# Performance work log

Measured on AMD Instinct MI355X. Metric: run time of the kernel, lower is better.

Reference implementation:

```python
import jax, jax.numpy as jnp
import numpy as np

D_IN, D, K, N_CLASSES = 384, 512, 6, 2
SCALE = D ** (-0.5)

def _linear_params(key, fan_in, fan_out):
    kw, kb = jax.random.split(key)
    w = jax.random.normal(kw, (fan_in, fan_out), jnp.float32) * 0.02
    b = jax.random.normal(kb, (fan_out,), jnp.float32) * 0.01
    return w, b

def setup_inputs() -> dict:
    key = jax.random.key(0)
    ks = jax.random.split(key, 10)
    x = jax.random.normal(ks[0], (16384, D_IN), jnp.float32)
    fc1_w, fc1_b = _linear_params(ks[1], D_IN, D)
    wh_w, wh_b = _linear_params(ks[2], D, D)
    wt_w, wt_b = _linear_params(ks[3], D, D)
    lin1_w, lin1_b = _linear_params(ks[4], D, D)
    lin2_w, lin2_b = _linear_params(ks[5], D, D)
    att1_w, att1_b = _linear_params(ks[6], D, D // 2)
    att2_w, att2_b = _linear_params(ks[7], D // 2, 1)
    ln_g = jnp.ones((D,), jnp.float32)
    ln_b = jnp.zeros((D,), jnp.float32)
    fc_w, fc_b = _linear_params(ks[8], D, N_CLASSES)
    return dict(x=x, fc1_w=fc1_w, fc1_b=fc1_b, wh_w=wh_w, wh_b=wh_b,
                wt_w=wt_w, wt_b=wt_b, lin1_w=lin1_w, lin1_b=lin1_b,
                lin2_w=lin2_w, lin2_b=lin2_b, att1_w=att1_w, att1_b=att1_b,
                att2_w=att2_w, att2_b=att2_b, ln_g=ln_g, ln_b=ln_b,
                fc_w=fc_w, fc_b=fc_b)

def _forward(x, fc1_w, fc1_b, wh_w, wh_b, wt_w, wt_b, lin1_w, lin1_b,
             lin2_w, lin2_b, att1_w, att1_b, att2_w, att2_b, ln_g, ln_b,
             fc_w, fc_b):
    lrelu = jax.nn.leaky_relu  # slope 0.01, matches nn.LeakyReLU default
    h = lrelu(x @ fc1_w + fc1_b)                    # [N, D]
    h = (h + h.mean(axis=0, keepdims=True)) * 0.5
    e_h = h @ wh_w + wh_b                           # [N, D]
    e_t = h @ wt_w + wt_b                           # [N, D]
    attn_logit = (e_h * SCALE) @ e_t.T              # [N, N]
    topk_w, topk_i = jax.lax.top_k(attn_logit, K)   # [N, K]
    Nb = e_t[topk_i]                                # gather neighbors [N, K, D]
    p = jax.nn.softmax(topk_w, axis=-1)             # [N, K]
    eh_r = p[..., None] * Nb + (1.0 - p)[..., None] * e_h[:, None, :]
    gate = jnp.tanh(e_h[:, None, :] + eh_r)         # [N, K, D]
    # faithful to torch.einsum('ijkl,ijkm->ijk', Nb, gate): product of sums
    ka_w = Nb.sum(axis=-1) * gate.sum(axis=-1)      # [N, K]
    ka_p = jax.nn.softmax(ka_w, axis=-1)
    e_Nh = jnp.einsum('nk,nkd->nd', ka_p, Nb)       # [N, D]
    sum_emb = lrelu((e_h + e_Nh) @ lin1_w + lin1_b)
    bi_emb = lrelu((e_h * e_Nh) @ lin2_w + lin2_b)
    emb = sum_emb + bi_emb                          # [N, D] (dropout=eval, identity)
    # GlobalAttention readout
    a = lrelu(emb @ att1_w + att1_b) @ att2_w + att2_b  # [N, 1]
    g = jax.nn.softmax(a, axis=0)
    pooled = (g * emb).sum(axis=0, keepdims=True)   # [1, D]
    mu = pooled.mean(axis=-1, keepdims=True)
    var = pooled.var(axis=-1, keepdims=True)
    normed = (pooled - mu) * jax.lax.rsqrt(var + 1e-5) * ln_g + ln_b
    logits = normed @ fc_w + fc_b                   # [1, n_classes]
    return logits

def reference(x, fc1_w, fc1_b, wh_w, wh_b, wt_w, wt_b, lin1_w, lin1_b,
              lin2_w, lin2_b, att1_w, att1_b, att2_w, att2_b, ln_g, ln_b,
              fc_w, fc_b):
    logits = _forward(x, fc1_w, fc1_b, wh_w, wh_b, wt_w, wt_b, lin1_w, lin1_b,
                      lin2_w, lin2_b, att1_w, att1_b, att2_w, att2_b,
                      ln_g, ln_b, fc_w, fc_b)
    y_prob = jax.nn.softmax(logits, axis=-1)
    return logits, y_prob
```

## Files before the change

kernel.cpp:

```cpp
#include <hip/hip_runtime.h>
#include <math.h>

#define NROWS 16384
#define DIN   384
#define DIM   512
#define KSEL  6
#define NSPLIT 4
#define COLS_PER_SPLIT (NROWS / NSPLIT)
#define ATT_SCALE 0.044194173824159216f

typedef unsigned short u16;
typedef __attribute__((ext_vector_type(8))) short bf16x8;
typedef __attribute__((ext_vector_type(16))) float f32x16;

static __device__ __forceinline__ float lrelu_f(float v) {
  return v > 0.f ? v : 0.01f * v;
}

static __device__ __forceinline__ u16 f2bf(float f) {
  unsigned u = __float_as_uint(f);
  unsigned r = (u + 0x7FFFu + ((u >> 16) & 1u)) >> 16;
  return (u16)r;
}

static __device__ __forceinline__ void sbar() {
  asm volatile("" ::: "memory");
  __builtin_amdgcn_s_barrier();
  asm volatile("" ::: "memory");
}

static __device__ __forceinline__ void wconv_body(const float* W, u16* Wt,
                                                  int K, int N, int t) {
  if (t >= K * N) return;
  int k = t / N, n = t - k * N;
  Wt[(size_t)n * K + k] = f2bf(W[t]);
}

__global__ __launch_bounds__(256)
void prep(const float* __restrict__ X, u16* __restrict__ Xb,
          const float* __restrict__ fc1_w, u16* __restrict__ fc1t,
          const float* __restrict__ wh_w, u16* __restrict__ wht,
          const float* __restrict__ wt_w, u16* __restrict__ wtt,
          const float* __restrict__ lin1_w, u16* __restrict__ lin1t,
          const float* __restrict__ lin2_w, u16* __restrict__ lin2t,
          const float* __restrict__ att1_w, u16* __restrict__ att1t) {
  const int b = blockIdx.x, tid = threadIdx.x;
  if (b < 3072) {
    int i = b * 256 + tid;
    const float4* p = (const float4*)X + (size_t)i * 2;
    float4 a = p[0], c = p[1];
    uint4 o;
    o.x = f2bf(a.x) | ((unsigned)f2bf(a.y) << 16);
    o.y = f2bf(a.z) | ((unsigned)f2bf(a.w) << 16);
    o.z = f2bf(c.x) | ((unsigned)f2bf(c.y) << 16);
    o.w = f2bf(c.z) | ((unsigned)f2bf(c.w) << 16);
    ((uint4*)Xb)[i] = o;
  } else if (b < 3840) {
    wconv_body(fc1_w, fc1t, 384, 512, (b - 3072) * 256 + tid);
  } else if (b < 4864) {
    wconv_body(wh_w, wht, 512, 512, (b - 3840) * 256 + tid);
  } else if (b < 5888) {
    wconv_body(wt_w, wtt, 512, 512, (b - 4864) * 256 + tid);
  } else if (b < 6912) {
    wconv_body(lin1_w, lin1t, 512, 512, (b - 5888) * 256 + tid);
  } else if (b < 7936) {
    wconv_body(lin2_w, lin2t, 512, 512, (b - 6912) * 256 + tid);
  } else {
    wconv_body(att1_w, att1t, 512, 256, (b - 7936) * 256 + tid);
  }
}

__global__ __launch_bounds__(256)
void colsum_partial(const float* __restrict__ H, float* __restrict__ part) {
  int col = blockIdx.x * 64 + (threadIdx.x & 63);
  int sub = threadIdx.x >> 6;
  int rEnd = blockIdx.y * 512 + 512;
  float s = 0.f;
  for (int r = blockIdx.y * 512 + sub; r < rEnd; r += 4)
    s += H[(size_t)r * DIM + col];
  __shared__ float sh[4][64];
  sh[sub][threadIdx.x & 63] = s;
  __syncthreads();
  if (threadIdx.x < 64) {
    float tot = sh[0][threadIdx.x] + sh[1][threadIdx.x] +
                sh[2][threadIdx.x] + sh[3][threadIdx.x];
    part[(size_t)blockIdx.y * DIM + col] = tot;
  }
}

__global__ void finalize_mean(const float* __restrict__ part,
                              float* __restrict__ mean) {
  int c = threadIdx.x;
  float s = 0.f;
  for (int j = 0; j < 32; j++) s += part[j * DIM + c];
  mean[c] = s * (1.0f / NROWS);
}

__global__ __launch_bounds__(256)
void h_fix_bf(const float* __restrict__ H0, const float* __restrict__ mean,
              u16* __restrict__ Hb) {
  int idx = blockIdx.x * 256 + threadIdx.x;
  int c = (idx * 8) & (DIM - 1);
  const float4* p = (const float4*)H0 + (size_t)idx * 2;
  float4 a = p[0], b = p[1];
  float4 m0 = *(const float4*)(mean + c);
  float4 m1 = *(const float4*)(mean + c + 4);
  a.x = (a.x + m0.x) * 0.5f; a.y = (a.y + m0.y) * 0.5f;
  a.z = (a.z + m0.z) * 0.5f; a.w = (a.w + m0.w) * 0.5f;
  b.x = (b.x + m1.x) * 0.5f; b.y = (b.y + m1.y) * 0.5f;
  b.z = (b.z + m1.z) * 0.5f; b.w = (b.w + m1.w) * 0.5f;
  uint4 o;
  o.x = f2bf(a.x) | ((unsigned)f2bf(a.y) << 16);
  o.y = f2bf(a.z) | ((unsigned)f2bf(a.w) << 16);
  o.z = f2bf(b.x) | ((unsigned)f2bf(b.y) << 16);
  o.w = f2bf(b.z) | ((unsigned)f2bf(b.w) << 16);
  ((uint4*)Hb)[idx] = o;
}

template<int ACT, int ACCUM, int STOREBF>
__global__ __launch_bounds__(256, 2)
void gemm_bf16(const u16* __restrict__ A, const u16* __restrict__ Wt,
               const float* __restrict__ bias, float* __restrict__ C,
               u16* __restrict__ Cb, float bscale, int K, int N) {
  __shared__ char lds[65536];
  const int tid = threadIdx.x;
  const int w = tid >> 6, l = tid & 63;
  const int l31 = l & 31, lh = l >> 5, lh16 = lh << 4;
  const int qg = w & 1, ng = w >> 1;
  const int swz = (l31 & 7) << 4;
  const int rowBase = blockIdx.y * 128;
  const int colBase = blockIdx.x * 128;
  const int nsteps = K >> 6;

  f32x16 z;
  #pragma unroll
  for (int i = 0; i < 16; i++) z[i] = 0.f;
  f32x16 acc00 = z, acc01 = z, acc10 = z, acc11 = z;

#define GSTAGE(buf_, kc_) do { \
    const int r_ = tid >> 3, j_ = tid & 7; \
    const int js_ = ((j_ ^ (r_ & 7)) << 3); \
    const u16* as_ = A + (size_t)rowBase * K + (kc_); \
    const u16* ws_ = Wt + (size_t)colBase * K + (kc_); \
    char* ab_ = lds + (buf_) * 16384; \
    char* wb_ = lds + 32768 + (buf_) * 16384; \
    _Pragma("unroll") \
    for (int p_ = 0; p_ < 4; ++p_) { \
      __builtin_amdgcn_global_load_lds( \
        (const __attribute__((address_space(1))) void*)(as_ + (size_t)(r_ + 32 * p_) * K + js_), \
        (__attribute__((address_space(3))) void*)(ab_ + w * 1024 + p_ * 4096), 16, 0, 0); \
      __builtin_amdgcn_global_load_lds( \
        (const __attribute__((address_space(1))) void*)(ws_ + (size_t)(r_ + 32 * p_) * K + js_), \
        (__attribute__((address_space(3))) void*)(wb_ + w * 1024 + p_ * 4096), 16, 0, 0); \
    } \
  } while (0)

  GSTAGE(0, 0);
  asm volatile("s_waitcnt vmcnt(0)" ::: "memory");
  sbar();
  #pragma unroll 1
  for (int s = 0; s < nsteps; ++s) {
    const int cur = s & 1;
    if (s + 1 < nsteps) GSTAGE(cur ^ 1, (s + 1) * 64);
    __builtin_amdgcn_sched_barrier(0);
    const char* ab = lds + cur * 16384;
    const char* wb = lds + 32768 + cur * 16384;
    __builtin_amdgcn_s_setprio(1);
    #pragma unroll
    for (int s4 = 0; s4 < 4; ++s4) {
      const int off = (s4 * 32 + lh16) ^ swz;
      bf16x8 am0 = *(const bf16x8*)(ab + (qg * 64 + l31) * 128 + off);
      bf16x8 am1 = *(const bf16x8*)(ab + (qg * 64 + 32 + l31) * 128 + off);
      bf16x8 wn0 = *(const bf16x8*)(wb + (ng * 64 + l31) * 128 + off);
      bf16x8 wn1 = *(const bf16x8*)(wb + (ng * 64 + 32 + l31) * 128 + off);
      acc00 = __builtin_amdgcn_mfma_f32_32x32x16_bf16(wn0, am0, acc00, 0, 0, 0);
      acc01 = __builtin_amdgcn_mfma_f32_32x32x16_bf16(wn1, am0, acc01, 0, 0, 0);
      acc10 = __builtin_amdgcn_mfma_f32_32x32x16_bf16(wn0, am1, acc10, 0, 0, 0);
      acc11 = __builtin_amdgcn_mfma_f32_32x32x16_bf16(wn1, am1, acc11, 0, 0, 0);
    }
    __builtin_amdgcn_s_setprio(0);
    asm volatile("s_waitcnt vmcnt(0)" ::: "memory");
    sbar();
  }
#undef GSTAGE

  float* Ls = (float*)lds;
  {
    const int m0 = qg * 64 + l31;
    const int k0 = (m0 & 7) << 2;
    #pragma unroll
    for (int r = 0; r < 16; ++r) {
      const int nd = ng * 64 + (r & 3) + 8 * (r >> 2) + 4 * lh;
      Ls[m0 * 128 + (nd ^ k0)] = acc00[r];
      Ls[m0 * 128 + ((nd + 32) ^ k0)] = acc01[r];
      Ls[(m0 + 32) * 128 + (nd ^ k0)] = acc10[r];
      Ls[(m0 + 32) * 128 + ((nd + 32) ^ k0)] = acc11[r];
    }
  }
  sbar();
  #pragma unroll
  for (int p = 0; p < 16; ++p) {
    int idx = tid + 256 * p;
    int m = idx >> 5, c4 = (idx & 31) << 2;
    float4 v = *(const float4*)&Ls[m * 128 + (c4 ^ ((m & 7) << 2))];
    int col = colBase + c4;
    float4 bv = *(const float4*)&bias[col];
    v.x += bv.x; v.y += bv.y; v.z += bv.z; v.w += bv.w;
    if (ACT) {
      v.x = lrelu_f(v.x); v.y = lrelu_f(v.y);
      v.z = lrelu_f(v.z); v.w = lrelu_f(v.w);
    }
    size_t o = (size_t)(rowBase + m) * N + col;
    if (ACCUM) {
      float4 c0 = *(const float4*)&C[o];
      v.x += c0.x; v.y += c0.y; v.z += c0.z; v.w += c0.w;
    }
    *(float4*)&C[o] = v;
    if (STOREBF) {
      ushort4 q;
      q.x = f2bf(v.x * bscale); q.y = f2bf(v.y * bscale);
      q.z = f2bf(v.z * bscale); q.w = f2bf(v.w * bscale);
      *(ushort4*)&Cb[o] = q;
    }
  }
}

#define T6(tv, tix, vv, cc) do { float v_ = (vv); \
  if (v_ > tv[5]) { tv[5] = v_; tix[5] = (cc); \
    if (tv[5] > tv[4]) { float t=tv[4];tv[4]=tv[5];tv[5]=t; int q=tix[4];tix[4]=tix[5];tix[5]=q; } \
    if (tv[4] > tv[3]) { float t=tv[3];tv[3]=tv[4];tv[4]=t; int q=tix[3];tix[3]=tix[4];tix[4]=q; } \
    if (tv[3] > tv[2]) { float t=tv[2];tv[2]=tv[3];tv[3]=t; int q=tix[2];tix[2]=tix[3];tix[3]=q; } \
    if (tv[2] > tv[1]) { float t=tv[1];tv[1]=tv[2];tv[2]=t; int q=tix[1];tix[1]=tix[2];tix[2]=q; } \
    if (tv[1] > tv[0]) { float t=tv[0];tv[0]=tv[1];tv[1]=t; int q=tix[0];tix[0]=tix[1];tix[1]=q; } \
  } } while (0)

__global__ __launch_bounds__(256, 2)
void attn_topk_mfma(const u16* __restrict__ EHb, const u16* __restrict__ ETb,
                    float* __restrict__ TWp, int* __restrict__ TIp) {
  __shared__ char lds[49152];
  const int tid = threadIdx.x;
  const int w = tid >> 6, l = tid & 63;
  const int l31 = l & 31, lh = l >> 5;

  const int bid = blockIdx.x;
  const int xcd = bid & 7;
  const int split = xcd & 3;
  const int rowBase = ((xcd >> 2) * 64 + (bid >> 3)) * 128;
  const int qrow = rowBase + w * 32 + l31;

  bf16x8 areg[32];
  {
    const u16* ap = EHb + (size_t)qrow * DIM + lh * 8;
    #pragma unroll
    for (int ks = 0; ks < 32; ++ks)
      areg[ks] = *(const bf16x8*)(ap + ks * 16);
  }

  f32x16 z;
  #pragma unroll
  for (int i = 0; i < 16; i++) z[i] = 0.f;
  f32x16 acc0 = z, acc1 = z;

  float tv[KSEL]; int tix[KSEL];
  #pragma unroll
  for (int k = 0; k < KSEL; k++) { tv[k] = -INFINITY; tix[k] = 0x7fffffff; }

#define STAGE(bufi_, ph_) do { \
    const int ct_ = (ph_) >> 2, kc_ = (ph_) & 3; \
    char* db_ = lds + (bufi_) * 16384; \
    const u16* bs_ = ETb + (size_t)(split * COLS_PER_SPLIT + ct_ * 64) * DIM + kc_ * 128; \
    _Pragma("unroll") \
    for (int p_ = 0; p_ < 4; ++p_) { \
      const int c_ = (w * 4 + p_) * 64 + l; \
      const int rn_ = c_ >> 4; \
      const int js_ = ((c_ & 15) ^ (rn_ & 15)) << 3; \
      __builtin_amdgcn_global_load_lds( \
        (const __attribute__((address_space(1))) void*)(bs_ + (size_t)rn_ * DIM + js_), \
        (__attribute__((address_space(3))) void*)(db_ + (w * 4 + p_) * 1024), 16, 0, 0); \
    } \
  } while (0)

  int bufr = 0;
  STAGE(0, 0);
  STAGE(1, 1);
  asm volatile("s_waitcnt vmcnt(4)" ::: "memory");

  #pragma unroll 1
  for (int ct = 0; ct < 64; ++ct) {
    #pragma unroll
    for (int kc = 0; kc < 4; ++kc) {
      sbar();
      const char* db = lds + bufr * 16384;
      __builtin_amdgcn_s_setprio(1);
      #pragma unroll
      for (int s = 0; s < 8; ++s) {
        const int j0 = ((s * 2 + lh) ^ (l31 & 15)) * 16;
        bf16x8 bn0 = *(const bf16x8*)(db + l31 * 256 + j0);
        const int r1 = 32 + l31;
        const int j1 = ((s * 2 + lh) ^ (r1 & 15)) * 16;
        bf16x8 bn1 = *(const bf16x8*)(db + r1 * 256 + j1);
        acc0 = __builtin_amdgcn_mfma_f32_32x32x16_bf16(bn0, areg[kc * 8 + s], acc0, 0, 0, 0);
        acc1 = __builtin_amdgcn_mfma_f32_32x32x16_bf16(bn1, areg[kc * 8 + s], acc1, 0, 0, 0);
      }
      __builtin_amdgcn_s_setprio(0);
      if (kc == 3) {
        const int cb = split * COLS_PER_SPLIT + ct * 64 + 4 * lh;
        #pragma unroll
        for (int r = 0; r < 16; ++r) {
          const int nd = cb + (r & 3) + 8 * (r >> 2);
          T6(tv, tix, acc0[r], nd);
          T6(tv, tix, acc1[r], nd + 32);
        }
        acc0 = z; acc1 = z;
      }
      __builtin_amdgcn_sched_barrier(0);
      {
        const int p = ct * 4 + kc;
        if (p + 2 < 256) {
          const int bs = (bufr >= 1) ? bufr - 1 : bufr + 2;
          STAGE(bs, p + 2);
        }
        if (p < 254) { asm volatile("s_waitcnt vmcnt(4)" ::: "memory"); }
        else         { asm volatile("s_waitcnt vmcnt(0)" ::: "memory"); }
      }
      bufr = (bufr == 2) ? 0 : bufr + 1;
    }
  }
#undef STAGE

  {
    float pv[KSEL]; int pi[KSEL];
    #pragma unroll
    for (int k = 0; k < KSEL; k++) {
      pv[k] = __shfl_xor(tv[k], 32);
      pi[k] = __shfl_xor(tix[k], 32);
    }
    #pragma unroll
    for (int k = 0; k < KSEL; k++) {
      float cv = pv[k]; int ci = pi[k];
      if ((cv > tv[5]) || (cv == tv[5] && ci < tix[5])) {
        tv[5] = cv; tix[5] = ci;
        if ((tv[5] > tv[4]) || (tv[5] == tv[4] && tix[5] < tix[4])) {
          float t = tv[4]; tv[4] = tv[5]; tv[5] = t;
          int q = tix[4]; tix[4] = tix[5]; tix[5] = q; }
        if ((tv[4] > tv[3]) || (tv[4] == tv[3] && tix[4] < tix[3])) {
          float t = tv[3]; tv[3] = tv[4]; tv[4] = t;
          int q = tix[3]; tix[3] = tix[4]; tix[4] = q; }
        if ((tv[3] > tv[2]) || (tv[3] == tv[2] && tix[3] < tix[2])) {
          float t = tv[2]; tv[2] = tv[3]; tv[3] = t;
          int q = tix[2]; tix[2] = tix[3]; tix[3] = q; }
        if ((tv[2] > tv[1]) || (tv[2] == tv[1] && tix[2] < tix[1])) {
          float t = tv[1]; tv[1] = tv[2]; tv[2] = t;
          int q = tix[1]; tix[1] = tix[2]; tix[2] = q; }
        if ((tv[1] > tv[0]) || (tv[1] == tv[0] && tix[1] < tix[0])) {
          float t = tv[0]; tv[0] = tv[1]; tv[1] = t;
          int q = tix[0]; tix[0] = tix[1]; tix[1] = q; }
      }
    }
  }
  if (lh == 0) {
    size_t o = ((size_t)split * NROWS + qrow) * KSEL;
    #pragma unroll
    for (int k = 0; k < KSEL; k++) { TWp[o + k] = tv[k]; TIp[o + k] = tix[k]; }
  }
}

__global__ __launch_bounds__(256)
void neighbor_kernel(const float* __restrict__ EH, const float* __restrict__ ET,
                     const float* __restrict__ TWp, const int* __restrict__ TIp,
                     u16* __restrict__ SINb, u16* __restrict__ BINb) {
  const int lane = threadIdx.x & 63;
  const int row = blockIdx.x * 4 + (threadIdx.x >> 6);
  const float* eh = EH + (size_t)row * DIM;
  float ehv[8];
  #pragma unroll
  for (int u = 0; u < 8; u++) ehv[u] = eh[u * 64 + lane];

  float tw[KSEL]; int ti[KSEL];
  #pragma unroll
  for (int k = 0; k < KSEL; k++) { tw[k] = -INFINITY; ti[k] = 0x7fffffff; }
  #pragma unroll
  for (int s = 0; s < NSPLIT; s++) {
    size_t o = ((size_t)s * NROWS + row) * KSEL;
    #pragma unroll
    for (int k = 0; k < KSEL; k++) {
      float cv = TWp[o + k]; int ci = TIp[o + k];
      if ((cv > tw[5]) || (cv == tw[5] && ci < ti[5])) {
        tw[5] = cv; ti[5] = ci;
        if ((tw[5] > tw[4]) || (tw[5] == tw[4] && ti[5] < ti[4])) {
          float t = tw[4]; tw[4] = tw[5]; tw[5] = t;
          int q = ti[4]; ti[4] = ti[5]; ti[5] = q; }
        if ((tw[4] > tw[3]) || (tw[4] == tw[3] && ti[4] < ti[3])) {
          float t = tw[3]; tw[3] = tw[4]; tw[4] = t;
          int q = ti[3]; ti[3] = ti[4]; ti[4] = q; }
        if ((tw[3] > tw[2]) || (tw[3] == tw[2] && ti[3] < ti[2])) {
          float t = tw[2]; tw[2] = tw[3]; tw[3] = t;
          int q = ti[2]; ti[2] = ti[3]; ti[3] = q; }
        if ((tw[2] > tw[1]) || (tw[2] == tw[1] && ti[2] < ti[1])) {
          float t = tw[1]; tw[1] = tw[2]; tw[2] = t;
          int q = ti[1]; ti[1] = ti[2]; ti[2] = q; }
        if ((tw[1] > tw[0]) || (tw[1] == tw[0] && ti[1] < ti[0])) {
          float t = tw[0]; tw[0] = tw[1]; tw[1] = t;
          int q = ti[0]; ti[0] = ti[1]; ti[1] = q; }
      }
    }
  }

  float m = tw[0];
  #pragma unroll
  for (int k = 1; k < KSEL; k++) m = fmaxf(m, tw[k]);
  float p[KSEL], ps = 0.f;
  #pragma unroll
  for (int k = 0; k < KSEL; k++) { p[k] = expf(tw[k] - m); ps += p[k]; }
  float inv = 1.f / ps;
  #pragma unroll
  for (int k = 0; k < KSEL; k++) p[k] *= inv;

  float nb[KSEL][8];
  float kaw[KSEL];
  #pragma unroll
  for (int k = 0; k < KSEL; k++) {
    const float* et = ET + (size_t)ti[k] * DIM;
    float snb = 0.f, sg = 0.f;
    #pragma unroll
    for (int u = 0; u < 8; u++) {
      float nbv = et[u * 64 + lane];
      nb[k][u] = nbv;
      float ehr = p[k] * nbv + (1.f - p[k]) * ehv[u];
      float g = tanhf(ehv[u] + ehr);
      snb += nbv; sg += g;
    }
    #pragma unroll
    for (int off = 32; off > 0; off >>= 1) {
      snb += __shfl_xor(snb, off);
      sg  += __shfl_xor(sg, off);
    }
    kaw[k] = snb * sg;
  }
  float km = kaw[0];
  #pragma unroll
  for (int k = 1; k < KSEL; k++) km = fmaxf(km, kaw[k]);
  float kp[KSEL], ks = 0.f;
  #pragma unroll
  for (int k = 0; k < KSEL; k++) { kp[k] = expf(kaw[k] - km); ks += kp[k]; }
  float kinv = 1.f / ks;
  #pragma unroll
  for (int k = 0; k < KSEL; k++) kp[k] *= kinv;

  #pragma unroll
  for (int u = 0; u < 8; u++) {
    float enh = 0.f;
    #pragma unroll
    for (int k = 0; k < KSEL; k++) enh += kp[k] * nb[k][u];
    size_t o = (size_t)row * DIM + u * 64 + lane;
    SINb[o] = f2bf(ehv[u] + enh);
    BINb[o] = f2bf(ehv[u] * enh);
  }
}

__global__ __launch_bounds__(256)
void att2_kernel(const float* __restrict__ HID, const float* __restrict__ w2,
                 const float* __restrict__ b2, float* __restrict__ ASC) {
  const int lane = threadIdx.x & 63;
  const int row = blockIdx.x * 4 + (threadIdx.x >> 6);
  float4 hv = ((const float4*)(HID + (size_t)row * 256))[lane];
  float4 wv = ((const float4*)w2)[lane];
  float s = hv.x * wv.x + hv.y * wv.y + hv.z * wv.z + hv.w * wv.w;
  #pragma unroll
  for (int off = 32; off > 0; off >>= 1) s += __shfl_xor(s, off);
  if (lane == 0) ASC[row] = s + b2[0];
}

__global__ __launch_bounds__(1024)
void areduce(const float* __restrict__ ASC, float* __restrict__ stats) {
  __shared__ float sm[1024];
  int t = threadIdx.x;
  float m = -INFINITY;
  for (int i = t; i < NROWS; i += 1024) m = fmaxf(m, ASC[i]);
  sm[t] = m; __syncthreads();
  for (int s = 512; s > 0; s >>= 1) {
    if (t < s) sm[t] = fmaxf(sm[t], sm[t + s]);
    __syncthreads();
  }
  float mx = sm[0]; __syncthreads();
  float sum = 0.f;
  for (int i = t; i < NROWS; i += 1024) sum += expf(ASC[i] - mx);
  sm[t] = sum; __syncthreads();
  for (int s = 512; s > 0; s >>= 1) {
    if (t < s) sm[t] += sm[t + s];
    __syncthreads();
  }
  if (t == 0) { stats[0] = mx; stats[1] = sm[0]; }
}

__global__ __launch_bounds__(256)
void pooled_partial(const float* __restrict__ EMB, const float* __restrict__ ASC,
                    const float* __restrict__ stats, float* __restrict__ part) {
  int col = blockIdx.x * 64 + (threadIdx.x & 63);
  int sub = threadIdx.x >> 6;
  float mx = stats[0];
  int rEnd = blockIdx.y * 512 + 512;
  float s = 0.f;
  for (int r = blockIdx.y * 512 + sub; r < rEnd; r += 4)
    s += expf(ASC[r] - mx) * EMB[(size_t)r * DIM + col];
  __shared__ float sh[4][64];
  sh[sub][threadIdx.x & 63] = s;
  __syncthreads();
  if (threadIdx.x < 64) {
    float tot = sh[0][threadIdx.x] + sh[1][threadIdx.x] +
                sh[2][threadIdx.x] + sh[3][threadIdx.x];
    part[(size_t)blockIdx.y * DIM + col] = tot;
  }
}

__global__ __launch_bounds__(512)
void final_kernel(const float* __restrict__ part, const float* __restrict__ stats,
                  const float* __restrict__ ln_g, const float* __restrict__ ln_b,
                  const float* __restrict__ fc_w, const float* __restrict__ fc_b,
                  float* __restrict__ out) {
  __shared__ float sh[512];
  int t = threadIdx.x;
  float s = 0.f;
  for (int j = 0; j < 32; j++) s += part[j * DIM + t];
  float pooled = s / stats[1];
  sh[t] = pooled; __syncthreads();
  for (int off = 256; off > 0; off >>= 1) {
    if (t < off) sh[t] += sh[t + off];
    __syncthreads();
  }
  float mu = sh[0] * (1.f / DIM); __syncthreads();
  float dv = pooled - mu;
  sh[t] = dv * dv; __syncthreads();
  for (int off = 256; off > 0; off >>= 1) {
    if (t < off) sh[t] += sh[t + off];
    __syncthreads();
  }
  float var = sh[0] * (1.f / DIM); __syncthreads();
  float normed = dv * rsqrtf(var + 1e-5f) * ln_g[t] + ln_b[t];
  sh[t] = normed * fc_w[t * 2 + 0]; __syncthreads();
  for (int off = 256; off > 0; off >>= 1) {
    if (t < off) sh[t] += sh[t + off];
    __syncthreads();
  }
  float l0 = sh[0] + fc_b[0]; __syncthreads();
  sh[t] = normed * fc_w[t * 2 + 1]; __syncthreads();
  for (int off = 256; off > 0; off >>= 1) {
    if (t < off) sh[t] += sh[t + off];
    __syncthreads();
  }
  float l1 = sh[0] + fc_b[1];
  if (t == 0) {
    float mm = fmaxf(l0, l1);
    float e0 = expf(l0 - mm), e1 = expf(l1 - mm);
    float si = 1.f / (e0 + e1);
    out[0] = l0; out[1] = l1; out[2] = e0 * si; out[3] = e1 * si;
  }
}

extern "C" void kernel_launch(void* const* d_in, const int* in_sizes, int n_in,
                              void* d_out, int out_size, void* d_ws, size_t ws_size,
                              hipStream_t stream) {
  (void)in_sizes; (void)n_in; (void)out_size; (void)ws_size;
  const float* x      = (const float*)d_in[0];
  const float* fc1_w  = (const float*)d_in[1];
  const float* fc1_b  = (const float*)d_in[2];
  const float* wh_w   = (const float*)d_in[3];
  const float* wh_b   = (const float*)d_in[4];
  const float* wt_w   = (const float*)d_in[5];
  const float* wt_b   = (const float*)d_in[6];
  const float* lin1_w = (const float*)d_in[7];
  const float* lin1_b = (const float*)d_in[8];
  const float* lin2_w = (const float*)d_in[9];
  const float* lin2_b = (const float*)d_in[10];
  const float* att1_w = (const float*)d_in[11];
  const float* att1_b = (const float*)d_in[12];
  const float* att2_w = (const float*)d_in[13];
  const float* att2_b = (const float*)d_in[14];
  const float* ln_g   = (const float*)d_in[15];
  const float* ln_b   = (const float*)d_in[16];
  const float* fc_w   = (const float*)d_in[17];
  const float* fc_b   = (const float*)d_in[18];
  float* out = (float*)d_out;

  char* ws = (char*)d_ws;
  float* B0   = (float*)(ws);
  float* B1   = (float*)(ws + 33554432);
  float* B2   = (float*)(ws + 67108864);
  float* TWp  = (float*)(ws + 100663296);
  int*   TIp  = (int*)  (ws + 100663296 + 1572864);
  float* part = (float*)(ws + 100663296 + 3145728 + 786432);
  float* mean = (float*)(ws + 100663296 + 3145728 + 786432 + 65536);
  float* ascr = (float*)(ws + 100663296 + 3145728 + 786432 + 65536 + 2048);
  float* stats= (float*)(ws + 100663296 + 3145728 + 786432 + 65536 + 2048 + 65536);
  u16*   hb   = (u16*)(ws + 104732672);
  u16*   EHb  = (u16*)(ws + 104732672 + 16777216);
  u16*   ETb  = (u16*)(ws + 104732672 + 33554432);
  u16*   WT   = (u16*)(ws + 104732672 + 50331648);
  u16* fc1t = WT;
  u16* wht  = fc1t + 196608;
  u16* wtt  = wht + 262144;
  u16* lin1t= wtt + 262144;
  u16* lin2t= lin1t + 262144;
  u16* att1t= lin2t + 262144;
  u16* xb   = (u16*)B1;
  u16* sinb = EHb;
  u16* binb = ETb;
  u16* embb = hb;

  prep<<<8448, 256, 0, stream>>>(x, xb, fc1_w, fc1t, wh_w, wht, wt_w, wtt,
                                 lin1_w, lin1t, lin2_w, lin2t, att1_w, att1t);
  gemm_bf16<1,0,0><<<dim3(4,128), 256, 0, stream>>>(xb, fc1t, fc1_b, B0, nullptr, 1.f, 384, 512);
  colsum_partial<<<dim3(8,32), 256, 0, stream>>>(B0, part);
  finalize_mean<<<1, 512, 0, stream>>>(part, mean);
  h_fix_bf<<<4096, 256, 0, stream>>>(B0, mean, hb);
  gemm_bf16<0,0,1><<<dim3(4,128), 256, 0, stream>>>(hb, wht, wh_b, B1, EHb, ATT_SCALE, 512, 512);
  gemm_bf16<0,0,1><<<dim3(4,128), 256, 0, stream>>>(hb, wtt, wt_b, B2, ETb, 1.f, 512, 512);
  attn_topk_mfma<<<512, 256, 0, stream>>>(EHb, ETb, TWp, TIp);
  neighbor_kernel<<<4096, 256, 0, stream>>>(B1, B2, TWp, TIp, sinb, binb);
  gemm_bf16<1,0,0><<<dim3(4,128), 256, 0, stream>>>(sinb, lin1t, lin1_b, B2, nullptr, 1.f, 512, 512);
  gemm_bf16<1,1,1><<<dim3(4,128), 256, 0, stream>>>(binb, lin2t, lin2_b, B2, embb, 1.f, 512, 512);
  gemm_bf16<1,0,0><<<dim3(2,128), 256, 0, stream>>>(embb, att1t, att1_b, B0, nullptr, 1.f, 512, 256);
  att2_kernel<<<4096, 256, 0, stream>>>(B0, att2_w, att2_b, ascr);
  areduce<<<1, 1024, 0, stream>>>(ascr, stats);
  pooled_partial<<<dim3(8,32), 256, 0, stream>>>(B2, ascr, stats, part);
  final_kernel<<<1, 512, 0, stream>>>(part, stats, ln_g, ln_b, fc_w, fc_b, out);
}
```

Baseline: 602.8 us.

## Split top-k attention columns into eight chunks with double-buffered LDS

The attention/top-k kernel now divides each column split into two halves, doubling the grid to 1024 blocks. LDS staging drops from triple to double buffering (32 KB), and launch bounds ask for three blocks per CU to raise occupancy. Each block also remaps its row tile by XCD. The neighbor kernel merges eight partial top-k lists instead of four, and the partial buffers move into the free B0 region. In exchange, each block reloads its query rows for twice as many blocks, the prefetch depth shrinks to one stage with a full vmcnt wait per step, and 1024 blocks at three per CU may leave an uneven tail wave.

```diff
diff --git a/kernel.cpp b/kernel.cpp
--- a/kernel.cpp
+++ b/kernel.cpp
@@ -234,18 +234,23 @@
     if (tv[1] > tv[0]) { float t=tv[0];tv[0]=tv[1];tv[1]=t; int q=tix[0];tix[0]=tix[1];tix[1]=q; } \
   } } while (0)
 
-__global__ __launch_bounds__(256, 2)
+__global__ __launch_bounds__(256, 3)
 void attn_topk_mfma(const u16* __restrict__ EHb, const u16* __restrict__ ETb,
                     float* __restrict__ TWp, int* __restrict__ TIp) {
-  __shared__ char lds[49152];
+  __shared__ char lds[32768];
   const int tid = threadIdx.x;
   const int w = tid >> 6, l = tid & 63;
   const int l31 = l & 31, lh = l >> 5;
 
   const int bid = blockIdx.x;
   const int xcd = bid & 7;
-  const int split = xcd & 3;
-  const int rowBase = ((xcd >> 2) * 64 + (bid >> 3)) * 128;
+  const int rem = bid >> 3;
+  const int rowTileL = rem & 15;
+  const int sc = rem >> 4;
+  const int split = sc & 3;
+  const int ch = sc >> 2;
+  const int rowBase = (xcd * 16 + rowTileL) * 128;
+  const int colBase0 = split * COLS_PER_SPLIT + ch * 2048;
   const int qrow = rowBase + w * 32 + l31;
 
   bf16x8 areg[32];
@@ -268,7 +273,7 @@
 #define STAGE(bufi_, ph_) do { \
     const int ct_ = (ph_) >> 2, kc_ = (ph_) & 3; \
     char* db_ = lds + (bufi_) * 16384; \
-    const u16* bs_ = ETb + (size_t)(split * COLS_PER_SPLIT + ct_ * 64) * DIM + kc_ * 128; \
+    const u16* bs_ = ETb + (size_t)(colBase0 + ct_ * 64) * DIM + kc_ * 128; \
     _Pragma("unroll") \
     for (int p_ = 0; p_ < 4; ++p_) { \
       const int c_ = (w * 4 + p_) * 64 + l; \
@@ -280,17 +285,18 @@
     } \
   } while (0)
 
-  int bufr = 0;
   STAGE(0, 0);
-  STAGE(1, 1);
-  asm volatile("s_waitcnt vmcnt(4)" ::: "memory");
+  asm volatile("s_waitcnt vmcnt(0)" ::: "memory");
 
   #pragma unroll 1
-  for (int ct = 0; ct < 64; ++ct) {
+  for (int ct = 0; ct < 32; ++ct) {
     #pragma unroll
     for (int kc = 0; kc < 4; ++kc) {
+      const int p = ct * 4 + kc;
       sbar();
-      const char* db = lds + bufr * 16384;
+      if (p + 1 < 128) STAGE((p + 1) & 1, p + 1);
+      __builtin_amdgcn_sched_barrier(0);
+      const char* db = lds + (p & 1) * 16384;
       __builtin_amdgcn_s_setprio(1);
       #pragma unroll
       for (int s = 0; s < 8; ++s) {
@@ -304,7 +310,7 @@
       }
       __builtin_amdgcn_s_setprio(0);
       if (kc == 3) {
-        const int cb = split * COLS_PER_SPLIT + ct * 64 + 4 * lh;
+        const int cb = colBase0 + ct * 64 + 4 * lh;
         #pragma unroll
         for (int r = 0; r < 16; ++r) {
           const int nd = cb + (r & 3) + 8 * (r >> 2);
@@ -314,16 +320,7 @@
         acc0 = z; acc1 = z;
       }
       __builtin_amdgcn_sched_barrier(0);
-      {
-        const int p = ct * 4 + kc;
-        if (p + 2 < 256) {
-          const int bs = (bufr >= 1) ? bufr - 1 : bufr + 2;
-          STAGE(bs, p + 2);
-        }
-        if (p < 254) { asm volatile("s_waitcnt vmcnt(4)" ::: "memory"); }
-        else         { asm volatile("s_waitcnt vmcnt(0)" ::: "memory"); }
-      }
-      bufr = (bufr == 2) ? 0 : bufr + 1;
+      asm volatile("s_waitcnt vmcnt(0)" ::: "memory");
     }
   }
 #undef STAGE
@@ -359,7 +356,7 @@
     }
   }
   if (lh == 0) {
-    size_t o = ((size_t)split * NROWS + qrow) * KSEL;
+    size_t o = ((size_t)(split * 2 + ch) * NROWS + qrow) * KSEL;
     #pragma unroll
     for (int k = 0; k < KSEL; k++) { TWp[o + k] = tv[k]; TIp[o + k] = tix[k]; }
   }
@@ -380,7 +377,7 @@
   #pragma unroll
   for (int k = 0; k < KSEL; k++) { tw[k] = -INFINITY; ti[k] = 0x7fffffff; }
   #pragma unroll
-  for (int s = 0; s < NSPLIT; s++) {
+  for (int s = 0; s < 8; s++) {
     size_t o = ((size_t)s * NROWS + row) * KSEL;
     #pragma unroll
     for (int k = 0; k < KSEL; k++) {
@@ -586,8 +583,6 @@
   float* B0   = (float*)(ws);
   float* B1   = (float*)(ws + 33554432);
   float* B2   = (float*)(ws + 67108864);
-  float* TWp  = (float*)(ws + 100663296);
-  int*   TIp  = (int*)  (ws + 100663296 + 1572864);
   float* part = (float*)(ws + 100663296 + 3145728 + 786432);
   float* mean = (float*)(ws + 100663296 + 3145728 + 786432 + 65536);
   float* ascr = (float*)(ws + 100663296 + 3145728 + 786432 + 65536 + 2048);
@@ -606,6 +601,8 @@
   u16* sinb = EHb;
   u16* binb = ETb;
   u16* embb = hb;
+  float* TWp = B0;
+  int*   TIp = (int*)(ws + 8 * (size_t)NROWS * KSEL * 4);
 
   prep<<<8448, 256, 0, stream>>>(x, xb, fc1_w, fc1t, wh_w, wht, wt_w, wtt,
                                  lin1_w, lin1t, lin2_w, lin2t, att1_w, att1t);
@@ -615,7 +612,7 @@
   h_fix_bf<<<4096, 256, 0, stream>>>(B0, mean, hb);
   gemm_bf16<0,0,1><<<dim3(4,128), 256, 0, stream>>>(hb, wht, wh_b, B1, EHb, ATT_SCALE, 512, 512);
   gemm_bf16<0,0,1><<<dim3(4,128), 256, 0, stream>>>(hb, wtt, wt_b, B2, ETb, 1.f, 512, 512);
-  attn_topk_mfma<<<512, 256, 0, stream>>>(EHb, ETb, TWp, TIp);
+  attn_topk_mfma<<<1024, 256, 0, stream>>>(EHb, ETb, TWp, TIp);
   neighbor_kernel<<<4096, 256, 0, stream>>>(B1, B2, TWp, TIp, sinb, binb);
   gemm_bf16<1,0,0><<<dim3(4,128), 256, 0, stream>>>(sinb, lin1t, lin1_b, B2, nullptr, 1.f, 512, 512);
   gemm_bf16<1,1,1><<<dim3(4,128), 256, 0, stream>>>(binb, lin2t, lin2_b, B2, embb, 1.f, 512, 512);
```

New measurement: 925.7 us. +53.6%, slower.
